# Kernel optimization log

Measured on AMD Instinct MI355X. Metric: run time of the kernel, lower is better.

Reference implementation:

```python
import jax, jax.numpy as jnp
import numpy as np

B, S, D, H = 4, 2048, 768, 12
HD = D // H  # head_dim = 64


def setup_inputs() -> dict:
    key = jax.random.key(0)
    k1, k2, k3, k4, k5 = jax.random.split(key, 5)
    scale = 0.02
    return {
        "x": jax.random.normal(k1, (B, S, D), dtype=jnp.float32),
        "w_qkv": jax.random.normal(k2, (D, 3 * D), dtype=jnp.float32) * scale,
        "b_qkv": jax.random.normal(k3, (3 * D,), dtype=jnp.float32) * scale,
        "w_proj": jax.random.normal(k4, (D, D), dtype=jnp.float32) * scale,
        "b_proj": jax.random.normal(k5, (D,), dtype=jnp.float32) * scale,
    }


def reference(x, w_qkv, b_qkv, w_proj, b_proj):
    b, s, d = x.shape
    # fused qkv projection: (b, s, 3d) -> (3, b, h, s, hd)
    qkv = x @ w_qkv + b_qkv
    qkv = qkv.reshape(b, s, 3, H, HD).transpose(2, 0, 3, 1, 4)
    q, k, v = qkv[0], qkv[1], qkv[2]
    # scaled dot-product attention with explicit (b, h, s, s) scores
    scores = jnp.einsum("bhqd,bhkd->bhqk", q, k) / jnp.sqrt(jnp.float32(HD))
    attn = jax.nn.softmax(scores, axis=-1)
    out = jnp.einsum("bhqk,bhkd->bhqd", attn, v)
    out = out.transpose(0, 2, 1, 3).reshape(b, s, d)  # concat heads
    return out @ w_proj + b_proj
```

## Files before the change

kernel.cpp:

```cpp
#include <hip/hip_runtime.h>
#include <hip/hip_bf16.h>
#include <stdint.h>


typedef __attribute__((ext_vector_type(8))) short bf16x8;
typedef __attribute__((ext_vector_type(4))) float f32x4;
typedef __attribute__((ext_vector_type(4))) unsigned short u16x4;

__device__ __forceinline__ unsigned short f2bf(float x) {
  union { float f; uint32_t u; } v; v.f = x;
  uint32_t r = v.u + 0x7FFF + ((v.u >> 16) & 1);
  return (unsigned short)(r >> 16);
}

__device__ __forceinline__ uint32_t cvtpk_bf16(float lo, float hi) {
  uint32_t r;
  asm("v_cvt_pk_bf16_f32 %0, %1, %2" : "=v"(r) : "v"(lo), "v"(hi));
  return r;
}

__device__ __forceinline__ void gload_lds16(const void* g, void* l) {
  __builtin_amdgcn_global_load_lds(
      (const __attribute__((address_space(1))) void*)g,
      (__attribute__((address_space(3))) void*)l, 16, 0, 0);
}

__device__ __forceinline__ void transpose_tile(const float* __restrict__ W,
                                               unsigned short* __restrict__ Wt,
                                               int K, int N, int k0, int n0,
                                               float (*tile)[65], int t) {
#pragma unroll
  for (int i = 0; i < 16; i++) {
    int idx = i * 256 + t; int r = idx >> 6, c = idx & 63;
    tile[r][c] = W[(size_t)(k0 + r) * N + n0 + c];
  }
  __syncthreads();
#pragma unroll
  for (int i = 0; i < 16; i++) {
    int idx = i * 256 + t; int r = idx >> 6, c = idx & 63;
    Wt[(size_t)(n0 + r) * K + k0 + c] = f2bf(tile[c][r]);
  }
}

__global__ void prep_kernel(const float* __restrict__ x,
                            unsigned short* __restrict__ xb,
                            const float* __restrict__ w_qkv,
                            unsigned short* __restrict__ wqt,
                            const float* __restrict__ w_proj,
                            unsigned short* __restrict__ wpt) {
  __shared__ float tile[64][65];
  const int id = blockIdx.x, t = threadIdx.x;
  if (id < 6144) {
    int idx = (id * 256 + t) * 4;
    f32x4 v = *(const f32x4*)(x + idx);
    u16x4 o;
    o[0] = f2bf(v[0]); o[1] = f2bf(v[1]); o[2] = f2bf(v[2]); o[3] = f2bf(v[3]);
    *(u16x4*)(xb + idx) = o;
  } else if (id < 6576) {
    int tid = id - 6144;
    transpose_tile(w_qkv, wqt, 768, 2304, (tid / 36) * 64, (tid % 36) * 64,
                   tile, t);
  } else {
    int tid = id - 6576;
    transpose_tile(w_proj, wpt, 768, 768, (tid / 12) * 64, (tid % 12) * 64,
                   tile, t);
  }
}

template <int EPI>
__global__ __launch_bounds__(256, 2) void gemm_kernel(
    const unsigned short* __restrict__ A,
    const unsigned short* __restrict__ Bt,
    const float* __restrict__ bias,
    void* __restrict__ out0,
    unsigned short* __restrict__ Kb,
    unsigned short* __restrict__ Vt,
    int M, int N, int K) {
  __shared__ unsigned short As[128 * 64];
  __shared__ unsigned short Bs[128 * 64];
  const int tid = threadIdx.x;
  const int wave = tid >> 6, lane = tid & 63;
  const int wm = wave >> 1, wn = wave & 1;
  const int id = blockIdx.x;
  const int xcd = id & 7, slot = id >> 3;
  int m0, n0;
  if (EPI == 0) {
    m0 = (xcd * 8 + slot / 18) * 128;
    n0 = (slot % 18) * 128;
  } else {
    m0 = (xcd * 8 + slot / 6) * 128;
    n0 = (slot % 6) * 128;
  }
  const int g = lane >> 4, c16 = lane & 15;
  f32x4 acc[4][4] = {};

  for (int k0 = 0; k0 < K; k0 += 64) {
    int rb = wave * 32;
#pragma unroll
    for (int j = 0; j < 4; j++) {
      int r = rb + j * 8 + (lane >> 3);
      int ca = (lane & 7) ^ (r & 7);
      gload_lds16(A + (size_t)(m0 + r) * K + k0 + ca * 8, As + (rb + j * 8) * 64);
      gload_lds16(Bt + (size_t)(n0 + r) * K + k0 + ca * 8, Bs + (rb + j * 8) * 64);
    }
    __syncthreads();
#pragma unroll
    for (int ks = 0; ks < 2; ks++) {
      bf16x8 af[4], bfr[4];
#pragma unroll
      for (int mi = 0; mi < 4; mi++) {
        int row = wm * 64 + mi * 16 + c16;
        int ch = (ks * 4 + g) ^ (row & 7);
        af[mi] = *(const bf16x8*)(As + row * 64 + ch * 8);
      }
#pragma unroll
      for (int nj = 0; nj < 4; nj++) {
        int row = wn * 64 + nj * 16 + c16;
        int ch = (ks * 4 + g) ^ (row & 7);
        bfr[nj] = *(const bf16x8*)(Bs + row * 64 + ch * 8);
      }
#pragma unroll
      for (int mi = 0; mi < 4; mi++)
#pragma unroll
        for (int nj = 0; nj < 4; nj++)
          acc[mi][nj] = __builtin_amdgcn_mfma_f32_16x16x32_bf16(
              af[mi], bfr[nj], acc[mi][nj], 0, 0, 0);
    }
    __syncthreads();
  }

  if (EPI == 0) {
    const float QSC = 0.125f * 1.44269504088896f;
    unsigned short* Qb = (unsigned short*)out0;
#pragma unroll
    for (int nj = 0; nj < 4; nj++) {
      int n = n0 + wn * 64 + nj * 16 + c16;
      int t = n / 768, rr = n % 768;
      int h = rr >> 6, d = rr & 63;
      float bv = bias[n];
#pragma unroll
      for (int mi = 0; mi < 4; mi++) {
        int mrow = m0 + wm * 64 + mi * 16 + g * 4;
        int b = mrow >> 11, s = mrow & 2047;
        if (t == 0) {
          size_t base = ((size_t)(b * 12 + h) * 2048 + s) * 64 + d;
#pragma unroll
          for (int rg = 0; rg < 4; rg++)
            Qb[base + (size_t)rg * 64] = f2bf((acc[mi][nj][rg] + bv) * QSC);
        } else if (t == 1) {
          size_t base = ((size_t)(b * 12 + h) * 2048 + s) * 64 + d;
#pragma unroll
          for (int rg = 0; rg < 4; rg++)
            Kb[base + (size_t)rg * 64] = f2bf(acc[mi][nj][rg] + bv);
        } else {
          int sp = (s & ~31) + (((s >> 2) & 3) << 3) + (((s >> 4) & 1) << 2);
          u16x4 p;
          p[0] = f2bf(acc[mi][nj][0] + bv);
          p[1] = f2bf(acc[mi][nj][1] + bv);
          p[2] = f2bf(acc[mi][nj][2] + bv);
          p[3] = f2bf(acc[mi][nj][3] + bv);
          *(u16x4*)(Vt + ((size_t)(b * 12 + h) * 64 + d) * 2048 + sp) = p;
        }
      }
    }
  } else {
    float* outp = (float*)out0;
#pragma unroll
    for (int nj = 0; nj < 4; nj++) {
      int n = n0 + wn * 64 + nj * 16 + c16;
      float bv = bias[n];
#pragma unroll
      for (int mi = 0; mi < 4; mi++) {
        int mrow = m0 + wm * 64 + mi * 16 + g * 4;
#pragma unroll
        for (int rg = 0; rg < 4; rg++)
          outp[(size_t)(mrow + rg) * N + n] = acc[mi][nj][rg] + bv;
      }
    }
  }
}

__global__ __launch_bounds__(256, 4) void attn_kernel(
    const unsigned short* __restrict__ Qb,
    const unsigned short* __restrict__ Kb,
    const unsigned short* __restrict__ Vt,
    unsigned short* __restrict__ Ao) {
  __shared__ unsigned short Ks[64 * 64];
  __shared__ unsigned short Vs[64 * 64];
  const int id = blockIdx.x;
  const int xcd = id & 7, slot = id >> 3;
  const int bh = xcd * 6 + (slot % 6);
  const int q0 = (slot / 6) * 128;
  const int tid = threadIdx.x;
  const int wave = tid >> 6, lane = tid & 63;
  const int g = lane >> 4, c16 = lane & 15;
  const int rw = c16 & 7;
  const int rb = wave * 16;

  const int sr = rb + (lane >> 3);
  const int sca = (lane & 7) ^ (sr & 7);
  const unsigned short* kp = Kb + ((size_t)bh * 2048 + sr) * 64 + sca * 8;
  const unsigned short* vp = Vt + ((size_t)bh * 64 + sr) * 2048 + sca * 8;

  bf16x8 qf[2][2];
  {
    const unsigned short* qp =
        Qb + ((size_t)bh * 2048 + q0 + wave * 32 + c16) * 64;
#pragma unroll
    for (int qa = 0; qa < 2; qa++) {
      qf[qa][0] = *(const bf16x8*)(qp + qa * 1024 + g * 8);
      qf[qa][1] = *(const bf16x8*)(qp + qa * 1024 + 32 + g * 8);
    }
  }
  f32x4 acc_o[2][4] = {};
  float l_run[2] = {0.f, 0.f};
  const int alane = (lane & 48) + g * 4;

  for (int kt = 0; kt < 32; kt++) {
    gload_lds16(kp, Ks + rb * 64);
    gload_lds16(kp + 8 * 64, Ks + (rb + 8) * 64);
    gload_lds16(vp, Vs + rb * 64);
    gload_lds16(vp + 8 * 2048, Vs + (rb + 8) * 64);
    kp += 64 * 64;
    vp += 64;
    __syncthreads();

    f32x4 sacc[2][4] = {};
#pragma unroll
    for (int ks = 0; ks < 2; ks++) {
#pragma unroll
      for (int nf = 0; nf < 4; nf++) {
        int row = nf * 16 + c16;
        int ch = (ks * 4 + g) ^ (row & 7);
        bf16x8 kf = *(const bf16x8*)(Ks + row * 64 + ch * 8);
        sacc[0][nf] =
            __builtin_amdgcn_mfma_f32_16x16x32_bf16(kf, qf[0][ks], sacc[0][nf], 0, 0, 0);
        sacc[1][nf] =
            __builtin_amdgcn_mfma_f32_16x16x32_bf16(kf, qf[1][ks], sacc[1][nf], 0, 0, 0);
      }
    }

#pragma unroll
    for (int qa = 0; qa < 2; qa++) {
      float rs = 0.f;
#pragma unroll
      for (int nf = 0; nf < 4; nf++) {
        sacc[qa][nf][0] = __builtin_amdgcn_exp2f(sacc[qa][nf][0]);
        sacc[qa][nf][1] = __builtin_amdgcn_exp2f(sacc[qa][nf][1]);
        sacc[qa][nf][2] = __builtin_amdgcn_exp2f(sacc[qa][nf][2]);
        sacc[qa][nf][3] = __builtin_amdgcn_exp2f(sacc[qa][nf][3]);
        rs += (sacc[qa][nf][0] + sacc[qa][nf][1]) +
              (sacc[qa][nf][2] + sacc[qa][nf][3]);
      }
      l_run[qa] += rs;
    }

#pragma unroll
    for (int ks = 0; ks < 2; ks++) {
      union { uint32_t w[4]; bf16x8 v8; } pa0, pa1;
      pa0.w[0] = cvtpk_bf16(sacc[0][2 * ks][0], sacc[0][2 * ks][1]);
      pa0.w[1] = cvtpk_bf16(sacc[0][2 * ks][2], sacc[0][2 * ks][3]);
      pa0.w[2] = cvtpk_bf16(sacc[0][2 * ks + 1][0], sacc[0][2 * ks + 1][1]);
      pa0.w[3] = cvtpk_bf16(sacc[0][2 * ks + 1][2], sacc[0][2 * ks + 1][3]);
      pa1.w[0] = cvtpk_bf16(sacc[1][2 * ks][0], sacc[1][2 * ks][1]);
      pa1.w[1] = cvtpk_bf16(sacc[1][2 * ks][2], sacc[1][2 * ks][3]);
      pa1.w[2] = cvtpk_bf16(sacc[1][2 * ks + 1][0], sacc[1][2 * ks + 1][1]);
      pa1.w[3] = cvtpk_bf16(sacc[1][2 * ks + 1][2], sacc[1][2 * ks + 1][3]);
#pragma unroll
      for (int nf = 0; nf < 4; nf++) {
        int row = nf * 16 + c16;
        int ch = (ks * 4 + g) ^ rw;
        bf16x8 vf = *(const bf16x8*)(&Vs[row * 64 + ch * 8]);
        acc_o[0][nf] =
            __builtin_amdgcn_mfma_f32_16x16x32_bf16(pa0.v8, vf, acc_o[0][nf], 0, 0, 0);
        acc_o[1][nf] =
            __builtin_amdgcn_mfma_f32_16x16x32_bf16(pa1.v8, vf, acc_o[1][nf], 0, 0, 0);
      }
    }
    __syncthreads();
  }

  const int b = bh / 12, h = bh % 12;
#pragma unroll
  for (int qa = 0; qa < 2; qa++) {
    float t = l_run[qa];
    t += __shfl_xor(t, 16);
    t += __shfl_xor(t, 32);
    float l_q[4];
#pragma unroll
    for (int rg = 0; rg < 4; rg++)
      l_q[rg] = __shfl(t, alane + rg);
#pragma unroll
    for (int nf = 0; nf < 4; nf++) {
#pragma unroll
      for (int rg = 0; rg < 4; rg++) {
        float v = acc_o[qa][nf][rg] / l_q[rg];
        int srow = q0 + wave * 32 + qa * 16 + g * 4 + rg;
        Ao[((size_t)(b * 2048 + srow)) * 768 + h * 64 + nf * 16 + c16] = f2bf(v);
      }
    }
  }
}

extern "C" void kernel_launch(void* const* d_in, const int* in_sizes, int n_in,
                              void* d_out, int out_size, void* d_ws, size_t ws_size,
                              hipStream_t stream) {
  const float* x      = (const float*)d_in[0];
  const float* w_qkv  = (const float*)d_in[1];
  const float* b_qkv  = (const float*)d_in[2];
  const float* w_proj = (const float*)d_in[3];
  const float* b_proj = (const float*)d_in[4];

  unsigned short* xb  = (unsigned short*)d_ws;
  unsigned short* wqt = xb + 6291456;
  unsigned short* wpt = wqt + 1769472;
  unsigned short* Qb  = wpt + 589824;
  unsigned short* Kb  = Qb + 6291456;
  unsigned short* Vt  = Kb + 6291456;
  unsigned short* Ao  = Vt + 6291456;

  prep_kernel<<<6720, 256, 0, stream>>>(x, xb, w_qkv, wqt, w_proj, wpt);

  gemm_kernel<0><<<1152, 256, 0, stream>>>(
      xb, wqt, b_qkv, (void*)Qb, Kb, Vt, 8192, 2304, 768);

  attn_kernel<<<768, 256, 0, stream>>>(Qb, Kb, Vt, Ao);

  gemm_kernel<1><<<384, 256, 0, stream>>>(
      Ao, wpt, b_proj, d_out, nullptr, nullptr, 8192, 768, 768);
}
```

Before: 135.3 us.

## Split attention over two key halves and add a reduction kernel

The attention kernel is split along the key dimension into two halves, doubling the grid from 768 to 1536 blocks. Each half writes an unnormalised bf16 partial output plus its row sums, and a new reduce kernel adds the two partials and divides by the combined sum. The second partial reuses the x workspace buffer, which is no longer needed at that point. The launch-bounds occupancy hint is also raised from 4 to 6. The goal is more parallelism and better CU fill, at the cost of an extra kernel launch, extra global traffic for the partials, and bf16 rounding of the partials before they are summed.

New measurement: 329.6 us. +143.5%, slower.

```diff
diff --git a/kernel.cpp b/kernel.cpp
--- a/kernel.cpp
+++ b/kernel.cpp
@@ -11,6 +11,11 @@
   union { float f; uint32_t u; } v; v.f = x;
   uint32_t r = v.u + 0x7FFF + ((v.u >> 16) & 1);
   return (unsigned short)(r >> 16);
+}
+
+__device__ __forceinline__ float bf2f(unsigned short u) {
+  union { uint32_t u; float f; } v; v.u = ((uint32_t)u) << 16;
+  return v.f;
 }
 
 __device__ __forceinline__ uint32_t cvtpk_bf16(float lo, float hi) {
@@ -180,17 +185,21 @@
   }
 }
 
-__global__ __launch_bounds__(256, 4) void attn_kernel(
+__global__ __launch_bounds__(256, 6) void attn_kernel(
     const unsigned short* __restrict__ Qb,
     const unsigned short* __restrict__ Kb,
     const unsigned short* __restrict__ Vt,
-    unsigned short* __restrict__ Ao) {
+    unsigned short* __restrict__ OutA,
+    unsigned short* __restrict__ OutB,
+    float* __restrict__ lbuf) {
   __shared__ unsigned short Ks[64 * 64];
   __shared__ unsigned short Vs[64 * 64];
   const int id = blockIdx.x;
   const int xcd = id & 7, slot = id >> 3;
   const int bh = xcd * 6 + (slot % 6);
-  const int q0 = (slot / 6) * 128;
+  const int rest = slot / 6;
+  const int q0 = (rest & 15) * 128;
+  const int half = rest >> 4;
   const int tid = threadIdx.x;
   const int wave = tid >> 6, lane = tid & 63;
   const int g = lane >> 4, c16 = lane & 15;
@@ -199,8 +208,10 @@
 
   const int sr = rb + (lane >> 3);
   const int sca = (lane & 7) ^ (sr & 7);
-  const unsigned short* kp = Kb + ((size_t)bh * 2048 + sr) * 64 + sca * 8;
-  const unsigned short* vp = Vt + ((size_t)bh * 64 + sr) * 2048 + sca * 8;
+  const unsigned short* kp =
+      Kb + ((size_t)bh * 2048 + half * 1024 + sr) * 64 + sca * 8;
+  const unsigned short* vp =
+      Vt + ((size_t)bh * 64 + sr) * 2048 + half * 1024 + sca * 8;
 
   bf16x8 qf[2][2];
   {
@@ -214,9 +225,8 @@
   }
   f32x4 acc_o[2][4] = {};
   float l_run[2] = {0.f, 0.f};
-  const int alane = (lane & 48) + g * 4;
-
-  for (int kt = 0; kt < 32; kt++) {
+
+  for (int kt = 0; kt < 16; kt++) {
     gload_lds16(kp, Ks + rb * 64);
     gload_lds16(kp + 8 * 64, Ks + (rb + 8) * 64);
     gload_lds16(vp, Vs + rb * 64);
@@ -280,26 +290,45 @@
     __syncthreads();
   }
 
+  unsigned short* outp = half ? OutB : OutA;
+  float* lp = lbuf + half * 98304;
   const int b = bh / 12, h = bh % 12;
 #pragma unroll
   for (int qa = 0; qa < 2; qa++) {
     float t = l_run[qa];
     t += __shfl_xor(t, 16);
     t += __shfl_xor(t, 32);
-    float l_q[4];
-#pragma unroll
-    for (int rg = 0; rg < 4; rg++)
-      l_q[rg] = __shfl(t, alane + rg);
+    if (lane < 16)
+      lp[bh * 2048 + q0 + wave * 32 + qa * 16 + c16] = t;
 #pragma unroll
     for (int nf = 0; nf < 4; nf++) {
 #pragma unroll
       for (int rg = 0; rg < 4; rg++) {
-        float v = acc_o[qa][nf][rg] / l_q[rg];
         int srow = q0 + wave * 32 + qa * 16 + g * 4 + rg;
-        Ao[((size_t)(b * 2048 + srow)) * 768 + h * 64 + nf * 16 + c16] = f2bf(v);
-      }
-    }
-  }
+        outp[((size_t)(b * 2048 + srow)) * 768 + h * 64 + nf * 16 + c16] =
+            f2bf(acc_o[qa][nf][rg]);
+      }
+    }
+  }
+}
+
+__global__ void reduce_attn_kernel(unsigned short* __restrict__ Oa,
+                                   const unsigned short* __restrict__ Ob,
+                                   const float* __restrict__ lbuf) {
+  const int t = blockIdx.x * 256 + threadIdx.x;
+  const int bh = t >> 15, rem = t & 32767;
+  const int s = rem >> 4, d4 = rem & 15;
+  const float linv =
+      1.0f / (lbuf[bh * 2048 + s] + lbuf[98304 + bh * 2048 + s]);
+  const int b = bh / 12, h = bh % 12;
+  size_t idx = ((size_t)(b * 2048 + s)) * 768 + h * 64 + d4 * 4;
+  u16x4 o0 = *(const u16x4*)(Oa + idx);
+  u16x4 o1 = *(const u16x4*)(Ob + idx);
+  u16x4 o;
+#pragma unroll
+  for (int j = 0; j < 4; j++)
+    o[j] = f2bf((bf2f(o0[j]) + bf2f(o1[j])) * linv);
+  *(u16x4*)(Oa + idx) = o;
 }
 
 extern "C" void kernel_launch(void* const* d_in, const int* in_sizes, int n_in,
@@ -318,13 +347,16 @@
   unsigned short* Kb  = Qb + 6291456;
   unsigned short* Vt  = Kb + 6291456;
   unsigned short* Ao  = Vt + 6291456;
+  float* lbuf = (float*)(Ao + 6291456);
 
   prep_kernel<<<6720, 256, 0, stream>>>(x, xb, w_qkv, wqt, w_proj, wpt);
 
   gemm_kernel<0><<<1152, 256, 0, stream>>>(
       xb, wqt, b_qkv, (void*)Qb, Kb, Vt, 8192, 2304, 768);
 
-  attn_kernel<<<768, 256, 0, stream>>>(Qb, Kb, Vt, Ao);
+  attn_kernel<<<1536, 256, 0, stream>>>(Qb, Kb, Vt, Ao, xb, lbuf);
+
+  reduce_attn_kernel<<<6144, 256, 0, stream>>>(Ao, xb, lbuf);
 
   gemm_kernel<1><<<384, 256, 0, stream>>>(
       Ao, wpt, b_proj, d_out, nullptr, nullptr, 8192, 768, 768);
```
